# Optimization experiments

Hardware: AMD Instinct MI355X
Metric: run time of the kernel (lower is better)

## Reference

```python
import jax, jax.numpy as jnp
import numpy as np

B, S, D, L = 16, 512, 256, 8192
DROP_P = 0.2


def setup_inputs() -> dict:
    key = jax.random.key(0)
    k1, k2, k3 = jax.random.split(key, 3)
    x = jax.random.normal(k1, (B, S, D), dtype=jnp.float32)
    label_emb = jax.random.normal(k2, (B, L, D), dtype=jnp.float32)
    mask = jax.random.uniform(k3, (B, S)) < 0.9
    return {"x": x, "mask": mask, "label_emb": label_emb}


def reference(x, mask, label_emb):
    # scores = x @ label_emb^T : [B, S, L]
    scores = jnp.einsum("bsd,bld->bsl", x, label_emb)
    # softmax over label dim (last)
    probs = jax.nn.softmax(scores, axis=-1)
    # post-softmax token masking (non-standard order, faithful to original)
    probs = jnp.where(mask[:, :, None], probs, jnp.zeros((), probs.dtype))
    # dropout (training=True in original), deterministic key for reproducibility
    keep = jax.random.bernoulli(jax.random.key(42), 1.0 - DROP_P, probs.shape)
    probs = jnp.where(keep, probs / (1.0 - DROP_P), jnp.zeros((), probs.dtype))
    # attention pooling: scores^T @ x : [B, L, D]
    return jnp.einsum("bsl,bsd->bld", probs, x)
```

## Files before the change

### kernel.cpp

```cpp
#include <hip/hip_runtime.h>
#include <stdint.h>
#include <stddef.h>

#define B_ 16
#define S_ 512
#define D_ 256
#define L_ 8192

typedef unsigned short u16;
typedef _Float16 f16;
typedef f16 f16x4 __attribute__((ext_vector_type(4)));
typedef f16 f16x8 __attribute__((ext_vector_type(8)));
typedef float f32x4 __attribute__((ext_vector_type(4)));

__device__ __forceinline__ void gl16(const void* g, void* l) {
  __builtin_amdgcn_global_load_lds(
      (const __attribute__((address_space(1))) unsigned int*)g,
      (__attribute__((address_space(3))) unsigned int*)l, 16, 0, 0);
}

__device__ __forceinline__ uint32_t rotl32(uint32_t x, int r) {
  return (x << r) | (x >> (32 - r));
}
__device__ __forceinline__ bool drop_keep(uint32_t j) {
  const uint32_t k0 = 0u, k1 = 42u, k2 = 0x1BD11BDAu ^ k0 ^ k1;
  uint32_t v0 = 0u + k0;
  uint32_t v1 = j + k1;
#define TF_R(r) { v0 += v1; v1 = rotl32(v1, (r)); v1 ^= v0; }
  TF_R(13) TF_R(15) TF_R(26) TF_R(6)
  v0 += k1; v1 += k2 + 1u;
  TF_R(17) TF_R(29) TF_R(16) TF_R(24)
  v0 += k2; v1 += k0 + 2u;
  TF_R(13) TF_R(15) TF_R(26) TF_R(6)
  v0 += k0; v1 += k1 + 3u;
  TF_R(17) TF_R(29) TF_R(16) TF_R(24)
  v0 += k1; v1 += k2 + 4u;
  TF_R(13) TF_R(15) TF_R(26) TF_R(6)
  v0 += k2; v1 += k0 + 5u;
#undef TF_R
  uint32_t bits = v0 ^ v1;
  float u = __uint_as_float((bits >> 9) | 0x3f800000u) - 1.0f;
  return u < 0.8f;
}

__global__ __launch_bounds__(256)
void conv16_kernel(const float* __restrict__ src, f16* __restrict__ dst, int n) {
  int i = (blockIdx.x * 256 + threadIdx.x) * 8;
  if (i >= n) return;
  float4 a = *(const float4*)&src[i];
  float4 b = *(const float4*)&src[i + 4];
  f16x8 o;
  o[0] = (f16)a.x; o[1] = (f16)a.y; o[2] = (f16)a.z; o[3] = (f16)a.w;
  o[4] = (f16)b.x; o[5] = (f16)b.y; o[6] = (f16)b.z; o[7] = (f16)b.w;
  *(f16x8*)&dst[i] = o;
}

__global__ __launch_bounds__(256)
void xt16_kernel(const float* __restrict__ x, f16* __restrict__ xT) {
  const int b = blockIdx.z, sb = blockIdx.x * 32, db = blockIdx.y * 32;
  __shared__ float t[32][33];
  const int tid = threadIdx.x;
  const int r = tid >> 3, c4 = (tid & 7) * 4;
  float4 v = *(const float4*)&x[((size_t)b * S_ + sb + r) * D_ + db + c4];
  t[r][c4] = v.x; t[r][c4 + 1] = v.y; t[r][c4 + 2] = v.z; t[r][c4 + 3] = v.w;
  __syncthreads();
  const int dr = tid >> 3, s4 = (tid & 7) * 4;
  f16x4 o;
#pragma unroll
  for (int j = 0; j < 4; ++j) o[j] = (f16)t[s4 + j][dr];
  *(f16x4*)&xT[((size_t)b * D_ + db + dr) * S_ + sb + s4] = o;
}

__global__ __launch_bounds__(256)
void gemm1t_f16(const f16* __restrict__ eh, const f16* __restrict__ xh,
                float* __restrict__ scoresT, float2* __restrict__ partials) {
  __shared__ __align__(16) f16 As[2][4096];
  __shared__ __align__(16) f16 Bs[2][4096];
  __shared__ float pmaxA[128][2];
  __shared__ float psumA[128][2];

  const int tid = threadIdx.x;
  const int lane = tid & 63, wave = tid >> 6;
  const int b = blockIdx.z, lt = blockIdx.x * 128, st = blockIdx.y * 128;

  const int lm = lane & 15, kq = lane >> 4;
  const int wm = (wave & 1) * 64, wn = (wave >> 1) * 64;

  const int c0 = wave * 2;
  auto stage = [&](int bi, int k0) {
#pragma unroll
    for (int i = 0; i < 2; ++i) {
      const int c = c0 + i, kqc = c >> 1, rb = (c & 1) * 64;
      gl16(eh + ((size_t)b * L_ + lt + rb + lane) * D_ + k0 + kqc * 8,
           (char*)As[bi] + c * 1024 + lane * 16);
      gl16(xh + ((size_t)b * S_ + st + rb + lane) * D_ + k0 + kqc * 8,
           (char*)Bs[bi] + c * 1024 + lane * 16);
    }
  };

  f32x4 acc[4][4] = {};

  stage(0, 0);
  __syncthreads();
  int bi = 0;
  for (int t = 0; t < 8; ++t) {
    if (t < 7) stage(bi ^ 1, (t + 1) * 32);
    f16x8 fa[4], fb[4];
#pragma unroll
    for (int mi = 0; mi < 4; ++mi)
      fa[mi] = *(const f16x8*)&As[bi][(kq * 128 + wm + mi * 16 + lm) * 8];
#pragma unroll
    for (int ni = 0; ni < 4; ++ni)
      fb[ni] = *(const f16x8*)&Bs[bi][(kq * 128 + wn + ni * 16 + lm) * 8];
#pragma unroll
    for (int mi = 0; mi < 4; ++mi)
#pragma unroll
      for (int ni = 0; ni < 4; ++ni)
        acc[mi][ni] = __builtin_amdgcn_mfma_f32_16x16x32_f16(
            fa[mi], fb[ni], acc[mi][ni], 0, 0, 0);
    __syncthreads();
    bi ^= 1;
  }

#pragma unroll
  for (int mi = 0; mi < 4; ++mi)
#pragma unroll
    for (int ni = 0; ni < 4; ++ni) {
      const int l0 = wm + mi * 16 + kq * 4;
      const int s = wn + ni * 16 + lm;
      float* sp = scoresT + ((size_t)b * L_ + lt + l0) * S_ + st + s;
#pragma unroll
      for (int r = 0; r < 4; ++r) sp[(size_t)r * S_] = acc[mi][ni][r];
    }

  float cmax[4];
#pragma unroll
  for (int ni = 0; ni < 4; ++ni) {
    float v = acc[0][ni][0];
#pragma unroll
    for (int mi = 0; mi < 4; ++mi)
#pragma unroll
      for (int r = 0; r < 4; ++r) v = fmaxf(v, acc[mi][ni][r]);
    cmax[ni] = v;
  }
#pragma unroll
  for (int ni = 0; ni < 4; ++ni) {
    cmax[ni] = fmaxf(cmax[ni], __shfl_xor(cmax[ni], 16, 64));
    cmax[ni] = fmaxf(cmax[ni], __shfl_xor(cmax[ni], 32, 64));
  }
  if (kq == 0) {
#pragma unroll
    for (int ni = 0; ni < 4; ++ni) pmaxA[wn + ni * 16 + lm][wave & 1] = cmax[ni];
  }
  __syncthreads();
  float colm[4];
#pragma unroll
  for (int ni = 0; ni < 4; ++ni) {
    const int s = wn + ni * 16 + lm;
    colm[ni] = fmaxf(pmaxA[s][0], pmaxA[s][1]);
  }
  float psum[4] = {};
#pragma unroll
  for (int ni = 0; ni < 4; ++ni)
#pragma unroll
    for (int mi = 0; mi < 4; ++mi)
#pragma unroll
      for (int r = 0; r < 4; ++r)
        psum[ni] += __expf(acc[mi][ni][r] - colm[ni]);
#pragma unroll
  for (int ni = 0; ni < 4; ++ni) {
    psum[ni] += __shfl_xor(psum[ni], 16, 64);
    psum[ni] += __shfl_xor(psum[ni], 32, 64);
  }
  if (kq == 0) {
#pragma unroll
    for (int ni = 0; ni < 4; ++ni) psumA[wn + ni * 16 + lm][wave & 1] = psum[ni];
  }
  __syncthreads();
  if (tid < 128) {
    float m = fmaxf(pmaxA[tid][0], pmaxA[tid][1]);
    float Z = psumA[tid][0] + psumA[tid][1];
    partials[((size_t)b * 64 + blockIdx.x) * S_ + st + tid] = make_float2(m, Z);
  }
}

__global__ __launch_bounds__(256)
void combine_kernel(const float2* __restrict__ partials,
                    const int* __restrict__ mask, float2* __restrict__ stats) {
  const int idx = blockIdx.x * 256 + threadIdx.x;
  const int b = idx / S_, si = idx - b * S_;
  float m = -3.402823466e38f, Z = 0.f;
  for (int t = 0; t < 64; ++t) {
    float2 p = partials[((size_t)b * 64 + t) * S_ + si];
    if (p.x > m) {
      Z = Z * __expf(m - p.x) + p.y;
      m = p.x;
    } else {
      Z += p.y * __expf(p.x - m);
    }
  }
  float f = (mask[idx] != 0) ? (1.25f / Z) : 0.0f;
  stats[idx] = make_float2(m, f);
}

__global__ __launch_bounds__(512)
void gemm2_fused(const float* __restrict__ scoresT, const f16* __restrict__ xT,
                 const float2* __restrict__ stats, float* __restrict__ out) {
  __shared__ __align__(16) float Ss[2][4096];
  __shared__ __align__(16) f16 Bs[2][8192];
  __shared__ float2 stat_s[S_];

  const int tid = threadIdx.x;
  const int lane = tid & 63, wave = tid >> 6;
  const int b = blockIdx.z, lt = blockIdx.x * 128;

  stat_s[tid] = stats[b * S_ + tid];

  const int lm = lane & 15, kq = lane >> 4;
  const int l_loc = wave * 16 + lm;
  const uint32_t gbase =
      (uint32_t)(b * S_) * (uint32_t)L_ + (uint32_t)(lt + l_loc);

  const int c0 = wave * 2;
  auto stage = [&](int bi, int k0) {
#pragma unroll
    for (int i = 0; i < 2; ++i) {
      const int c = c0 + i;
      {
        const int gs = c >> 1, lb = (c & 1) * 64;
        gl16(scoresT + ((size_t)b * L_ + lt + lb + lane) * S_ + k0 + gs * 4,
             (char*)Ss[bi] + c * 1024 + lane * 16);
      }
      {
        const int kqc = c >> 2, db = (c & 3) * 64;
        gl16(xT + ((size_t)b * D_ + db + lane) * S_ + k0 + kqc * 8,
             (char*)Bs[bi] + c * 1024 + lane * 16);
      }
    }
  };

  f32x4 acc[16] = {};

  stage(0, 0);
  __syncthreads();
  int bi = 0;
  for (int k0 = 0; k0 < S_; k0 += 32) {
    if (k0 < S_ - 32) stage(bi ^ 1, k0 + 32);

    const f32x4 v0 = *(const f32x4*)&Ss[bi][((kq * 2 + 0) * 128 + l_loc) * 4];
    const f32x4 v1 = *(const f32x4*)&Ss[bi][((kq * 2 + 1) * 128 + l_loc) * 4];
    float pv[8];
#pragma unroll
    for (int j = 0; j < 4; ++j) {
      const float2 mf = stat_s[k0 + kq * 8 + j];
      pv[j] = __expf(v0[j] - mf.x) * mf.y;
    }
#pragma unroll
    for (int j = 0; j < 4; ++j) {
      const float2 mf = stat_s[k0 + kq * 8 + 4 + j];
      pv[4 + j] = __expf(v1[j] - mf.x) * mf.y;
    }
    f16x8 fa;
#pragma unroll
    for (int j = 0; j < 8; ++j) {
      const uint32_t gidx = gbase + (uint32_t)(k0 + kq * 8 + j) * (uint32_t)L_;
      fa[j] = drop_keep(gidx) ? (f16)pv[j] : (f16)0.f;
    }

#pragma unroll
    for (int ni = 0; ni < 16; ++ni) {
      const f16x8 fb = *(const f16x8*)&Bs[bi][(kq * 256 + ni * 16 + lm) * 8];
      acc[ni] = __builtin_amdgcn_mfma_f32_16x16x32_f16(fa, fb, acc[ni], 0, 0, 0);
    }
    __syncthreads();
    bi ^= 1;
  }

#pragma unroll
  for (int ni = 0; ni < 16; ++ni) {
    const int n = ni * 16 + lm;
    float* op = out + ((size_t)b * L_ + lt + wave * 16 + kq * 4) * D_ + n;
#pragma unroll
    for (int r = 0; r < 4; ++r) op[(size_t)r * D_] = acc[ni][r];
  }
}

extern "C" void kernel_launch(void* const* d_in, const int* in_sizes, int n_in,
                              void* d_out, int out_size, void* d_ws, size_t ws_size,
                              hipStream_t stream) {
  const float* x = (const float*)d_in[0];
  const int* mask = (const int*)d_in[1];
  const float* E = (const float*)d_in[2];
  float* out = (float*)d_out;

  char* ws = (char*)d_ws;
  const size_t nE = (size_t)B_ * L_ * D_;
  const size_t nX = (size_t)B_ * S_ * D_;
  size_t o = 0;
  f16* Eh = (f16*)(ws + o); o += nE * 2;
  f16* Xh = (f16*)(ws + o); o += nX * 2;
  f16* XT = (f16*)(ws + o); o += nX * 2;
  float2* stats = (float2*)(ws + o); o += (size_t)B_ * S_ * 8;
  float2* partials = (float2*)(ws + o); o += (size_t)B_ * 64 * S_ * 8;
  float* scoresT = (float*)(ws + o);

  conv16_kernel<<<dim3((unsigned)(nE / 8 / 256)), 256, 0, stream>>>(E, Eh, (int)nE);
  conv16_kernel<<<dim3((unsigned)(nX / 8 / 256)), 256, 0, stream>>>(x, Xh, (int)nX);
  xt16_kernel<<<dim3(S_ / 32, D_ / 32, B_), 256, 0, stream>>>(x, XT);

  gemm1t_f16<<<dim3(L_ / 128, S_ / 128, B_), 256, 0, stream>>>(
      Eh, Xh, scoresT, partials);
  combine_kernel<<<dim3(B_ * S_ / 256), 256, 0, stream>>>(partials, mask, stats);
  gemm2_fused<<<dim3(L_ / 128, 1, B_), 512, 0, stream>>>(scoresT, XT, stats, out);
}
```

Before: 612.1 us.

## Coalesce global-to-LDS staging and load scores directly to registers in gemm2

Changes the LDS staging layout in both GEMMs so that each 16-lane group loads 16 rows with four 16-byte K chunks per row, which makes global reads more contiguous per row, and the fragment reads are reindexed to match. In gemm2, the scoresT tile no longer goes through LDS. Each lane register-prefetches its own 8 floats for the next K step straight from global memory. This removes the Ss shared buffer and its bank traffic and lowers LDS use, in exchange for uncached per-lane global loads that may stall the exp/MFMA loop.

New measurement: 571.7 us. 1.07x faster.

```diff
diff --git a/kernel.cpp b/kernel.cpp
--- a/kernel.cpp
+++ b/kernel.cpp
@@ -85,15 +85,16 @@
 
   const int lm = lane & 15, kq = lane >> 4;
   const int wm = (wave & 1) * 64, wn = (wave >> 1) * 64;
-
-  const int c0 = wave * 2;
+  const int ca = (wave & 1) * 4, cb = (wave >> 1) * 4;
+
+  const int srow = lane & 15, sko = (lane >> 4) * 8;
   auto stage = [&](int bi, int k0) {
 #pragma unroll
     for (int i = 0; i < 2; ++i) {
-      const int c = c0 + i, kqc = c >> 1, rb = (c & 1) * 64;
-      gl16(eh + ((size_t)b * L_ + lt + rb + lane) * D_ + k0 + kqc * 8,
+      const int c = wave * 2 + i;
+      gl16(eh + ((size_t)b * L_ + lt + c * 16 + srow) * D_ + k0 + sko,
            (char*)As[bi] + c * 1024 + lane * 16);
-      gl16(xh + ((size_t)b * S_ + st + rb + lane) * D_ + k0 + kqc * 8,
+      gl16(xh + ((size_t)b * S_ + st + c * 16 + srow) * D_ + k0 + sko,
            (char*)Bs[bi] + c * 1024 + lane * 16);
     }
   };
@@ -108,10 +109,10 @@
     f16x8 fa[4], fb[4];
 #pragma unroll
     for (int mi = 0; mi < 4; ++mi)
-      fa[mi] = *(const f16x8*)&As[bi][(kq * 128 + wm + mi * 16 + lm) * 8];
+      fa[mi] = *(const f16x8*)&As[bi][((ca + mi) * 64 + kq * 16 + lm) * 8];
 #pragma unroll
     for (int ni = 0; ni < 4; ++ni)
-      fb[ni] = *(const f16x8*)&Bs[bi][(kq * 128 + wn + ni * 16 + lm) * 8];
+      fb[ni] = *(const f16x8*)&Bs[bi][((cb + ni) * 64 + kq * 16 + lm) * 8];
 #pragma unroll
     for (int mi = 0; mi < 4; ++mi)
 #pragma unroll
@@ -206,7 +207,6 @@
 __global__ __launch_bounds__(512)
 void gemm2_fused(const float* __restrict__ scoresT, const f16* __restrict__ xT,
                  const float2* __restrict__ stats, float* __restrict__ out) {
-  __shared__ __align__(16) float Ss[2][4096];
   __shared__ __align__(16) f16 Bs[2][8192];
   __shared__ float2 stat_s[S_];
 
@@ -221,44 +221,46 @@
   const uint32_t gbase =
       (uint32_t)(b * S_) * (uint32_t)L_ + (uint32_t)(lt + l_loc);
 
-  const int c0 = wave * 2;
+  const int srow = lane & 15, sko = (lane >> 4) * 8;
+  const size_t xb_base = (size_t)b * D_ * S_;
   auto stage = [&](int bi, int k0) {
 #pragma unroll
     for (int i = 0; i < 2; ++i) {
-      const int c = c0 + i;
-      {
-        const int gs = c >> 1, lb = (c & 1) * 64;
-        gl16(scoresT + ((size_t)b * L_ + lt + lb + lane) * S_ + k0 + gs * 4,
-             (char*)Ss[bi] + c * 1024 + lane * 16);
-      }
-      {
-        const int kqc = c >> 2, db = (c & 3) * 64;
-        gl16(xT + ((size_t)b * D_ + db + lane) * S_ + k0 + kqc * 8,
-             (char*)Bs[bi] + c * 1024 + lane * 16);
-      }
+      const int c = wave * 2 + i;
+      gl16(xT + xb_base + (size_t)(c * 16 + srow) * S_ + k0 + sko,
+           (char*)Bs[bi] + c * 1024 + lane * 16);
     }
   };
 
+  const float* srowp =
+      scoresT + ((size_t)b * L_ + lt + l_loc) * S_ + kq * 8;
+
   f32x4 acc[16] = {};
 
+  f32x4 sv0 = *(const f32x4*)&srowp[0];
+  f32x4 sv1 = *(const f32x4*)&srowp[4];
   stage(0, 0);
   __syncthreads();
   int bi = 0;
   for (int k0 = 0; k0 < S_; k0 += 32) {
-    if (k0 < S_ - 32) stage(bi ^ 1, k0 + 32);
-
-    const f32x4 v0 = *(const f32x4*)&Ss[bi][((kq * 2 + 0) * 128 + l_loc) * 4];
-    const f32x4 v1 = *(const f32x4*)&Ss[bi][((kq * 2 + 1) * 128 + l_loc) * 4];
+    f32x4 nv0, nv1;
+    const bool more = (k0 < S_ - 32);
+    if (more) {
+      stage(bi ^ 1, k0 + 32);
+      nv0 = *(const f32x4*)&srowp[k0 + 32];
+      nv1 = *(const f32x4*)&srowp[k0 + 36];
+    }
+
     float pv[8];
 #pragma unroll
     for (int j = 0; j < 4; ++j) {
       const float2 mf = stat_s[k0 + kq * 8 + j];
-      pv[j] = __expf(v0[j] - mf.x) * mf.y;
+      pv[j] = __expf(sv0[j] - mf.x) * mf.y;
     }
 #pragma unroll
     for (int j = 0; j < 4; ++j) {
       const float2 mf = stat_s[k0 + kq * 8 + 4 + j];
-      pv[4 + j] = __expf(v1[j] - mf.x) * mf.y;
+      pv[4 + j] = __expf(sv1[j] - mf.x) * mf.y;
     }
     f16x8 fa;
 #pragma unroll
@@ -269,10 +271,11 @@
 
 #pragma unroll
     for (int ni = 0; ni < 16; ++ni) {
-      const f16x8 fb = *(const f16x8*)&Bs[bi][(kq * 256 + ni * 16 + lm) * 8];
+      const f16x8 fb = *(const f16x8*)&Bs[bi][(ni * 64 + kq * 16 + lm) * 8];
       acc[ni] = __builtin_amdgcn_mfma_f32_16x16x32_f16(fa, fb, acc[ni], 0, 0, 0);
     }
     __syncthreads();
+    if (more) { sv0 = nv0; sv1 = nv1; }
     bi ^= 1;
   }
 
```
